# Kernel tuning notes

Hardware: AMD Instinct MI355X
Metric: run time of the kernel (lower is better)

Reference implementation:

```python
import jax, jax.numpy as jnp
import numpy as np

D_MODEL = 1024
STATE_DIM = 64
SEQ_L = 2048


def hippo_legs_A(N):
    n = jnp.arange(N, dtype=jnp.float32)
    two_n1 = 2.0 * n + 1.0
    sq = jnp.sqrt(two_n1[:, None] * two_n1[None, :])
    A = jnp.tril(sq, k=-1) * -1.0
    return A + jnp.diag(-(n + 1.0))


def setup_inputs() -> dict:
    key = jax.random.key(0)
    kB, kC = jax.random.split(key)
    N = STATE_DIM
    n = jnp.arange(N, dtype=jnp.float32)
    B_ref = jnp.sqrt(2.0 * n + 1.0)  # (N,)
    B = jnp.tile(B_ref[None, :], (D_MODEL, 1)) + 0.01 * jax.random.normal(kB, (D_MODEL, N), dtype=jnp.float32)
    C = 0.1 * jax.random.normal(kC, (D_MODEL, N), dtype=jnp.float32)
    D = jnp.zeros((D_MODEL,), dtype=jnp.float32)
    log_dt = jnp.log(jnp.asarray(0.1, dtype=jnp.float32))
    return {"B": B, "C": C, "D": D, "log_dt": log_dt, "L": SEQ_L}


def reference(B, C, D, log_dt, L):
    N = B.shape[1]
    A = hippo_legs_A(N)                       # (N,N) continuous-time HiPPO-LegS
    dt = jax.nn.softplus(log_dt) + 1e-06
    I = jnp.eye(N, dtype=A.dtype)
    lhs = I - 0.5 * dt * A
    rhs = I + 0.5 * dt * A
    A_bar = jnp.linalg.solve(lhs, rhs)        # (N,N) bilinear discretization
    B_bar = jnp.linalg.solve(lhs, (dt * B).T).T  # (d_model, N)
    A_bar_T = A_bar.T

    def step(x, _):
        y = jnp.sum(C * x, axis=-1)           # (d_model,)
        return x @ A_bar_T, y

    _, ys = jax.lax.scan(step, B_bar, None, length=L)  # ys: (L, d_model)
    K = ys.T                                   # (d_model, L)
    K = K.at[:, 0].add(D)
    return K[:, None, :]                       # (d_model, 1, L)
```

## Files before the change

### kernel.cpp

```cpp
#include <hip/hip_runtime.h>

typedef unsigned short ushort_t;
typedef unsigned int uint_t;
typedef short short8 __attribute__((ext_vector_type(8)));
typedef float f32x4 __attribute__((ext_vector_type(4)));

namespace {

template<int CTRL, int RM>
__device__ __forceinline__ float dpp_mov0(float v) {
  return __int_as_float(__builtin_amdgcn_update_dpp(
      0, __float_as_int(v), CTRL, RM, 0xF, false));
}
template<int CTRL, int RM>
__device__ __forceinline__ float dpp_mov1(float v) {
  return __int_as_float(__builtin_amdgcn_update_dpp(
      0x3f800000, __float_as_int(v), CTRL, RM, 0xF, false));
}

__device__ __forceinline__ float rl(float v, int k) {
  return __int_as_float(__builtin_amdgcn_readlane(__float_as_int(v), k));
}

struct Hoist {
  float cs0, cs1, cs2, cs3, cs4, cs5;
  float gs0, gs1, gs2, gs3, gs4, gs5;
  float r, inv_d, hr, alpha, k2;
};

__device__ __forceinline__ Hoist make_hoist(float dt, int n) {
  float h = 0.5f * dt, fn = (float)n;
  float r = sqrtf(2.f * fn + 1.f);
  float d = 1.f + h * (fn + 1.f);
  float inv_d = 1.f / d;
  float g = (1.f - h * fn) * inv_d;
  float c = g - 1.f;
  Hoist H;
  H.r = r; H.inv_d = inv_d; H.hr = h * r;
  H.alpha = 1.f + h * fn;
  H.k2 = r * (2.f - d) * inv_d;
#define COEF_STEP(IDX, CTRL, RM)                                        \
  H.cs##IDX = c; H.gs##IDX = g;                                         \
  { float cP = dpp_mov0<CTRL, RM>(c);                                   \
    float gP = dpp_mov1<CTRL, RM>(g);                                   \
    c = fmaf(g, cP, c); g = g * gP; }
  COEF_STEP(0, 0x111, 0xF)
  COEF_STEP(1, 0x112, 0xF)
  COEF_STEP(2, 0x114, 0xF)
  COEF_STEP(3, 0x118, 0xF)
  COEF_STEP(4, 0x142, 0xA)
  COEF_STEP(5, 0x143, 0xC)
#undef COEF_STEP
  return H;
}

__device__ __forceinline__ float abar_apply(float x, const Hoist& H) {
  float w1 = H.r * x, w2 = H.k2 * x;
#define APPLY_STEP(IDX, CTRL, RM)                                       \
  { float w1P = dpp_mov0<CTRL, RM>(w1);                                 \
    float w2P = dpp_mov0<CTRL, RM>(w2);                                 \
    w2 = fmaf(H.cs##IDX, w1P, fmaf(H.gs##IDX, w2P, w2));                \
    w1 += w1P; }
  APPLY_STEP(0, 0x111, 0xF)
  APPLY_STEP(1, 0x112, 0xF)
  APPLY_STEP(2, 0x114, 0xF)
  APPLY_STEP(3, 0x118, 0xF)
  APPLY_STEP(4, 0x142, 0xA)
  APPLY_STEP(5, 0x143, 0xC)
#undef APPLY_STEP
  float tp = dpp_mov0<0x138, 0xF>(w2);
  return H.inv_d * fmaf(-H.hr, w1 + tp, H.alpha * x);
}

template<int CTRL, int RM>
__device__ __forceinline__ void linrec_step(float& G, float& W) {
  float Wo = dpp_mov0<CTRL, RM>(W);
  float Go = dpp_mov1<CTRL, RM>(G);
  W = fmaf(G, Wo, W);
  G *= Go;
}
__device__ __forceinline__ float lhs_solve(float z, const Hoist& H) {
  float G = H.gs0, W = H.r * z * H.inv_d;
  linrec_step<0x111, 0xF>(G, W);
  linrec_step<0x112, 0xF>(G, W);
  linrec_step<0x114, 0xF>(G, W);
  linrec_step<0x118, 0xF>(G, W);
  linrec_step<0x142, 0xA>(G, W);
  linrec_step<0x143, 0xC>(G, W);
  float sp = dpp_mov0<0x138, 0xF>(W);
  return (z - H.hr * sp) * H.inv_d;
}

__device__ __forceinline__ float softplus_dt(float ldt) {
  return log1pf(expf(ldt)) + 1e-6f;
}

__device__ __forceinline__ void load_row_g(const float* __restrict__ base,
                                           float (&pc)[64]) {
  const float4* p4 = (const float4*)base;
  #pragma unroll
  for (int q = 0; q < 16; ++q) {
    float4 f = p4[q];
    pc[4*q+0] = f.x; pc[4*q+1] = f.y; pc[4*q+2] = f.z; pc[4*q+3] = f.w;
  }
}

__device__ __forceinline__ float qapply(const float (&pc)[64], float u) {
  float a0 = 0.f, a1 = 0.f, a2 = 0.f, a3 = 0.f;
  #pragma unroll
  for (int k = 0; k < 64; k += 4) {
    a0 = fmaf(pc[k + 0], rl(u, k + 0), a0);
    a1 = fmaf(pc[k + 1], rl(u, k + 1), a1);
    a2 = fmaf(pc[k + 2], rl(u, k + 2), a2);
    a3 = fmaf(pc[k + 3], rl(u, k + 3), a3);
  }
  return (a0 + a1) + (a2 + a3);
}

__device__ __forceinline__ float grow_matvec(const float* __restrict__ M,
                                             float u, int lane) {
  float a0 = 0.f, a1 = 0.f, a2 = 0.f, a3 = 0.f;
  const float4* m4 = (const float4*)(M + lane * 64);
  #pragma unroll
  for (int q = 0; q < 16; ++q) {
    float4 f = m4[q];
    a0 = fmaf(f.x, rl(u, 4 * q + 0), a0);
    a1 = fmaf(f.y, rl(u, 4 * q + 1), a1);
    a2 = fmaf(f.z, rl(u, 4 * q + 2), a2);
    a3 = fmaf(f.w, rl(u, 4 * q + 3), a3);
  }
  return (a0 + a1) + (a2 + a3);
}

__device__ __forceinline__ void split_store(float v, ushort_t* Hi,
                                            ushort_t* Lo, int row, int n) {
  uint_t uv = __float_as_uint(v);
  float hf = __uint_as_float(uv & 0xFFFF0000u);
  uint_t lv = __float_as_uint(v - hf);
  int idx = (row << 6) | (((n >> 3) ^ (row & 7)) << 3) | (n & 7);
  Hi[idx] = (ushort_t)(uv >> 16);
  Lo[idx] = (ushort_t)(lv >> 16);
}

__device__ __forceinline__ int frag_off(int row, int chunk) {
  return (row << 6) | ((chunk ^ (row & 7)) << 3);
}

}

__global__ __launch_bounds__(64) void hippo_pow(const float* __restrict__ ldt_p,
                                                float* __restrict__ A32c,
                                                float* __restrict__ QROW,
                                                float* __restrict__ Q2ROW) {
  const int lane = threadIdx.x;
  const int m = blockIdx.x;
  const float dt = softplus_dt(ldt_p[0]);
  const Hoist H = make_hoist(dt, lane);
  float x = (lane == m) ? 1.f : 0.f;
  #pragma unroll 1
  for (int s = 0; s < 32; ++s) x = abar_apply(x, H);
  A32c[lane * 64 + m] = x;
  #pragma unroll 1
  for (int s = 0; s < 32; ++s) x = abar_apply(x, H);
  QROW[m * 64 + lane] = x;
  #pragma unroll 1
  for (int s = 0; s < 64; ++s) x = abar_apply(x, H);
  Q2ROW[m * 64 + lane] = x;
}

__global__ __launch_bounds__(256, 2) void hippo_main(
    const float* __restrict__ B, const float* __restrict__ C,
    const float* __restrict__ Dv, const float* __restrict__ ldt_p,
    const float* __restrict__ A32c, const float* __restrict__ QROW,
    const float* __restrict__ Q2ROW, float* __restrict__ out,
    int NI, int L) {
  __shared__ __align__(16) ushort_t Uh[32 * 64], Ulo[32 * 64];
  __shared__ __align__(16) ushort_t Vh[64 * 64], Vlo[64 * 64];
  const int d = blockIdx.x;
  const int tau = threadIdx.x;
  const int lane = tau & 63;
  const int w = tau >> 6;
  const float dt = softplus_dt(ldt_p[0]);

  if (w == 0) {
    const Hoist H = make_hoist(dt, lane);
    float v = lhs_solve(dt * B[d * 64 + lane], H);
    #pragma unroll 1
    for (int j = 0; j < 32; ++j) {
      split_store(v, Vh, Vlo, j, lane);
      if (j < 31) v = abar_apply(v, H);
    }
  } else if (w == 3) {
    const Hoist H = make_hoist(dt, lane);
    float bb = lhs_solve(dt * B[d * 64 + lane], H);
    float v = grow_matvec(A32c, bb, lane);
    #pragma unroll 1
    for (int j = 32; j < 64; ++j) {
      split_store(v, Vh, Vlo, j, lane);
      if (j < 63) v = abar_apply(v, H);
    }
  } else if (w == 1) {
    float pc[64];
    load_row_g(Q2ROW + lane * 64, pc);
    float u = C[d * 64 + lane];
    #pragma unroll 1
    for (int a = 0; a < 16; ++a) {
      split_store(u, Uh, Ulo, 2 * a, lane);
      if (a < 15) u = qapply(pc, u);
    }
  } else {
    float pc[64];
    load_row_g(Q2ROW + lane * 64, pc);
    float u = grow_matvec(QROW, C[d * 64 + lane], lane);
    #pragma unroll 1
    for (int a = 0; a < 16; ++a) {
      split_store(u, Uh, Ulo, 2 * a + 1, lane);
      if (a < 15) u = qapply(pc, u);
    }
  }
  __syncthreads();

  const int it = w & 1;
  const int jp = w >> 1;
  const int arow = lane & 15;
  const int kg = lane >> 4;
  f32x4 acc0 = {0.f, 0.f, 0.f, 0.f};
  f32x4 acc1 = {0.f, 0.f, 0.f, 0.f};
  const int ia = (it << 4) + arow;
  const int jv0 = (jp << 5) + arow;
  const int jv1 = jv0 + 16;
  #pragma unroll
  for (int k0 = 0; k0 < 2; ++k0) {
    const int ci = (k0 << 2) + kg;
    short8 ah = *(const short8*)&Uh[frag_off(ia, ci)];
    short8 al = *(const short8*)&Ulo[frag_off(ia, ci)];
    short8 b0h = *(const short8*)&Vh[frag_off(jv0, ci)];
    short8 b0l = *(const short8*)&Vlo[frag_off(jv0, ci)];
    short8 b1h = *(const short8*)&Vh[frag_off(jv1, ci)];
    short8 b1l = *(const short8*)&Vlo[frag_off(jv1, ci)];
    acc0 = __builtin_amdgcn_mfma_f32_16x16x32_bf16(ah, b0h, acc0, 0, 0, 0);
    acc0 = __builtin_amdgcn_mfma_f32_16x16x32_bf16(al, b0h, acc0, 0, 0, 0);
    acc0 = __builtin_amdgcn_mfma_f32_16x16x32_bf16(ah, b0l, acc0, 0, 0, 0);
    acc1 = __builtin_amdgcn_mfma_f32_16x16x32_bf16(ah, b1h, acc1, 0, 0, 0);
    acc1 = __builtin_amdgcn_mfma_f32_16x16x32_bf16(al, b1h, acc1, 0, 0, 0);
    acc1 = __builtin_amdgcn_mfma_f32_16x16x32_bf16(ah, b1l, acc1, 0, 0, 0);
  }
  #pragma unroll
  for (int r = 0; r < 4; ++r) {
    const int i = (it << 4) + (kg << 2) + r;
    const int j0 = (jp << 5) + arow;
    float y0 = acc0[r];
    if (i == 0 && j0 == 0) y0 += Dv[d];
    out[((size_t)d << 11) + (i << 6) + j0] = y0;
    out[((size_t)d << 11) + (i << 6) + j0 + 16] = acc1[r];
  }
}

extern "C" void kernel_launch(void* const* d_in, const int* in_sizes, int n_in,
                              void* d_out, int out_size, void* d_ws, size_t ws_size,
                              hipStream_t stream) {
  const float* B   = (const float*)d_in[0];
  const float* C   = (const float*)d_in[1];
  const float* Dv  = (const float*)d_in[2];
  const float* ldt = (const float*)d_in[3];
  const int d_model = in_sizes[2];
  const int L = out_size / d_model;
  const int NI = L / 64;
  float* A32c  = (float*)d_ws;
  float* QROW  = (float*)d_ws + 4096;
  float* Q2ROW = (float*)d_ws + 8192;
  hippo_pow<<<64, 64, 0, stream>>>(ldt, A32c, QROW, Q2ROW);
  hippo_main<<<d_model, 256, 0, stream>>>(B, C, Dv, ldt, A32c, QROW, Q2ROW,
                                          (float*)d_out, NI, L);
}
```

Measured before the change: 39.38 us.

## Split each channel across two blocks by output column half

The grid doubles to two blocks per channel, and each block builds only 32 V vectors (half h uses A^32 times B_bar as its start) instead of 64. The MFMA stage per wave shrinks to one 16x16 tile, and the shared memory for V is halved. This adds parallelism and shortens the serial recurrence chain per block. In exchange, the U (C-side) powers are computed twice per channel, and wave 3 now sits idle during the build phase.

```diff
diff --git a/kernel.cpp b/kernel.cpp
--- a/kernel.cpp
+++ b/kernel.cpp
@@ -172,11 +172,11 @@
     const float* __restrict__ B, const float* __restrict__ C,
     const float* __restrict__ Dv, const float* __restrict__ ldt_p,
     const float* __restrict__ A32c, const float* __restrict__ QROW,
-    const float* __restrict__ Q2ROW, float* __restrict__ out,
-    int NI, int L) {
+    const float* __restrict__ Q2ROW, float* __restrict__ out) {
   __shared__ __align__(16) ushort_t Uh[32 * 64], Ulo[32 * 64];
-  __shared__ __align__(16) ushort_t Vh[64 * 64], Vlo[64 * 64];
-  const int d = blockIdx.x;
+  __shared__ __align__(16) ushort_t Vh[32 * 64], Vlo[32 * 64];
+  const int d = blockIdx.x >> 1;
+  const int h = blockIdx.x & 1;
   const int tau = threadIdx.x;
   const int lane = tau & 63;
   const int w = tau >> 6;
@@ -185,19 +185,11 @@
   if (w == 0) {
     const Hoist H = make_hoist(dt, lane);
     float v = lhs_solve(dt * B[d * 64 + lane], H);
+    if (h) v = grow_matvec(A32c, v, lane);
     #pragma unroll 1
     for (int j = 0; j < 32; ++j) {
       split_store(v, Vh, Vlo, j, lane);
       if (j < 31) v = abar_apply(v, H);
-    }
-  } else if (w == 3) {
-    const Hoist H = make_hoist(dt, lane);
-    float bb = lhs_solve(dt * B[d * 64 + lane], H);
-    float v = grow_matvec(A32c, bb, lane);
-    #pragma unroll 1
-    for (int j = 32; j < 64; ++j) {
-      split_store(v, Vh, Vlo, j, lane);
-      if (j < 63) v = abar_apply(v, H);
     }
   } else if (w == 1) {
     float pc[64];
@@ -208,7 +200,7 @@
       split_store(u, Uh, Ulo, 2 * a, lane);
       if (a < 15) u = qapply(pc, u);
     }
-  } else {
+  } else if (w == 2) {
     float pc[64];
     load_row_g(Q2ROW + lane * 64, pc);
     float u = grow_matvec(QROW, C[d * 64 + lane], lane);
@@ -221,38 +213,30 @@
   __syncthreads();
 
   const int it = w & 1;
-  const int jp = w >> 1;
+  const int jt = w >> 1;
   const int arow = lane & 15;
   const int kg = lane >> 4;
-  f32x4 acc0 = {0.f, 0.f, 0.f, 0.f};
-  f32x4 acc1 = {0.f, 0.f, 0.f, 0.f};
+  f32x4 acc = {0.f, 0.f, 0.f, 0.f};
   const int ia = (it << 4) + arow;
-  const int jv0 = (jp << 5) + arow;
-  const int jv1 = jv0 + 16;
+  const int jv = (jt << 4) + arow;
   #pragma unroll
   for (int k0 = 0; k0 < 2; ++k0) {
     const int ci = (k0 << 2) + kg;
     short8 ah = *(const short8*)&Uh[frag_off(ia, ci)];
     short8 al = *(const short8*)&Ulo[frag_off(ia, ci)];
-    short8 b0h = *(const short8*)&Vh[frag_off(jv0, ci)];
-    short8 b0l = *(const short8*)&Vlo[frag_off(jv0, ci)];
-    short8 b1h = *(const short8*)&Vh[frag_off(jv1, ci)];
-    short8 b1l = *(const short8*)&Vlo[frag_off(jv1, ci)];
-    acc0 = __builtin_amdgcn_mfma_f32_16x16x32_bf16(ah, b0h, acc0, 0, 0, 0);
-    acc0 = __builtin_amdgcn_mfma_f32_16x16x32_bf16(al, b0h, acc0, 0, 0, 0);
-    acc0 = __builtin_amdgcn_mfma_f32_16x16x32_bf16(ah, b0l, acc0, 0, 0, 0);
-    acc1 = __builtin_amdgcn_mfma_f32_16x16x32_bf16(ah, b1h, acc1, 0, 0, 0);
-    acc1 = __builtin_amdgcn_mfma_f32_16x16x32_bf16(al, b1h, acc1, 0, 0, 0);
-    acc1 = __builtin_amdgcn_mfma_f32_16x16x32_bf16(ah, b1l, acc1, 0, 0, 0);
+    short8 bh = *(const short8*)&Vh[frag_off(jv, ci)];
+    short8 bl = *(const short8*)&Vlo[frag_off(jv, ci)];
+    acc = __builtin_amdgcn_mfma_f32_16x16x32_bf16(ah, bh, acc, 0, 0, 0);
+    acc = __builtin_amdgcn_mfma_f32_16x16x32_bf16(al, bh, acc, 0, 0, 0);
+    acc = __builtin_amdgcn_mfma_f32_16x16x32_bf16(ah, bl, acc, 0, 0, 0);
   }
   #pragma unroll
   for (int r = 0; r < 4; ++r) {
     const int i = (it << 4) + (kg << 2) + r;
-    const int j0 = (jp << 5) + arow;
-    float y0 = acc0[r];
-    if (i == 0 && j0 == 0) y0 += Dv[d];
-    out[((size_t)d << 11) + (i << 6) + j0] = y0;
-    out[((size_t)d << 11) + (i << 6) + j0 + 16] = acc1[r];
+    const int jg = (h << 5) + (jt << 4) + arow;
+    float y = acc[r];
+    if (i == 0 && jg == 0) y += Dv[d];
+    out[((size_t)d << 11) + (i << 6) + jg] = y;
   }
 }
 
@@ -264,12 +248,10 @@
   const float* Dv  = (const float*)d_in[2];
   const float* ldt = (const float*)d_in[3];
   const int d_model = in_sizes[2];
-  const int L = out_size / d_model;
-  const int NI = L / 64;
   float* A32c  = (float*)d_ws;
   float* QROW  = (float*)d_ws + 4096;
   float* Q2ROW = (float*)d_ws + 8192;
   hippo_pow<<<64, 64, 0, stream>>>(ldt, A32c, QROW, Q2ROW);
-  hippo_main<<<d_model, 256, 0, stream>>>(B, C, Dv, ldt, A32c, QROW, Q2ROW,
-                                          (float*)d_out, NI, L);
-}
+  hippo_main<<<2 * d_model, 256, 0, stream>>>(B, C, Dv, ldt, A32c, QROW, Q2ROW,
+                                              (float*)d_out);
+}
```

After: 48.94 us. +24.3%, slower.

## Replace per-channel serial recurrences with precomputed matrix powers and batched GEMMs

Applied to the files above, without the earlier changes.

Precomputes all powers A_bar^1..63 and powers of A_bar^64 in small kernels, then computes the V and U sequences for all channels with a batched split-bf16 MFMA GEMM instead of serial per-channel matvec chains. The final output kernel reads V/U from global workspace instead of shared memory. This aims to remove the long serial dependency chain inside each block, at the cost of four launches, much larger workspace traffic (tens of MB written and re-read) and serial chains kept in the prep kernels.

```diff
diff --git a/kernel.cpp b/kernel.cpp
--- a/kernel.cpp
+++ b/kernel.cpp
@@ -117,127 +117,167 @@
   return (a0 + a1) + (a2 + a3);
 }
 
-__device__ __forceinline__ float grow_matvec(const float* __restrict__ M,
-                                             float u, int lane) {
-  float a0 = 0.f, a1 = 0.f, a2 = 0.f, a3 = 0.f;
-  const float4* m4 = (const float4*)(M + lane * 64);
-  #pragma unroll
-  for (int q = 0; q < 16; ++q) {
-    float4 f = m4[q];
-    a0 = fmaf(f.x, rl(u, 4 * q + 0), a0);
-    a1 = fmaf(f.y, rl(u, 4 * q + 1), a1);
-    a2 = fmaf(f.z, rl(u, 4 * q + 2), a2);
-    a3 = fmaf(f.w, rl(u, 4 * q + 3), a3);
-  }
-  return (a0 + a1) + (a2 + a3);
-}
-
-__device__ __forceinline__ void split_store(float v, ushort_t* Hi,
-                                            ushort_t* Lo, int row, int n) {
+__device__ __forceinline__ void bsplit(float v, ushort_t& h, ushort_t& l) {
   uint_t uv = __float_as_uint(v);
   float hf = __uint_as_float(uv & 0xFFFF0000u);
   uint_t lv = __float_as_uint(v - hf);
-  int idx = (row << 6) | (((n >> 3) ^ (row & 7)) << 3) | (n & 7);
-  Hi[idx] = (ushort_t)(uv >> 16);
-  Lo[idx] = (ushort_t)(lv >> 16);
-}
-
-__device__ __forceinline__ int frag_off(int row, int chunk) {
-  return (row << 6) | ((chunk ^ (row & 7)) << 3);
-}
-
-}
-
-__global__ __launch_bounds__(64) void hippo_pow(const float* __restrict__ ldt_p,
-                                                float* __restrict__ A32c,
-                                                float* __restrict__ QROW,
-                                                float* __restrict__ Q2ROW) {
+  h = (ushort_t)(uv >> 16);
+  l = (ushort_t)(lv >> 16);
+}
+
+}
+
+__global__ __launch_bounds__(64) void hippo_prep(
+    const float* __restrict__ B, const float* __restrict__ C,
+    const float* __restrict__ ldt_p, float* __restrict__ AjRM,
+    float* __restrict__ PRM, ushort_t* __restrict__ Bh, ushort_t* __restrict__ Bl,
+    ushort_t* __restrict__ Ch, ushort_t* __restrict__ Cl,
+    ushort_t* __restrict__ Vh, ushort_t* __restrict__ Vl,
+    ushort_t* __restrict__ Uh, ushort_t* __restrict__ Ul) {
+  const int lane = threadIdx.x;
+  const int bid = blockIdx.x;
+  const float dt = softplus_dt(ldt_p[0]);
+  const Hoist H = make_hoist(dt, lane);
+  if (bid < 64) {
+    const int m = bid;
+    float x = (lane == m) ? 1.f : 0.f;
+    #pragma unroll 1
+    for (int s = 1; s <= 64; ++s) {
+      x = abar_apply(x, H);
+      if (s < 64) AjRM[s * 4096 + lane * 64 + m] = x;
+      else        PRM[lane * 64 + m] = x;
+    }
+  } else {
+    const int d = bid - 64;
+    float bb = lhs_solve(dt * B[d * 64 + lane], H);
+    ushort_t h, l;
+    bsplit(bb, h, l);
+    Bh[d * 64 + lane] = h;               Bl[d * 64 + lane] = l;
+    Vh[(size_t)d * 4096 + lane] = h;     Vl[(size_t)d * 4096 + lane] = l;
+    float cc = C[d * 64 + lane];
+    bsplit(cc, h, l);
+    Ch[d * 64 + lane] = h;               Cl[d * 64 + lane] = l;
+    Uh[(size_t)d * 2048 + lane] = h;     Ul[(size_t)d * 2048 + lane] = l;
+  }
+}
+
+__global__ __launch_bounds__(64) void hippo_ppow(const float* __restrict__ PRM,
+                                                 float* __restrict__ PiT) {
   const int lane = threadIdx.x;
   const int m = blockIdx.x;
-  const float dt = softplus_dt(ldt_p[0]);
-  const Hoist H = make_hoist(dt, lane);
-  float x = (lane == m) ? 1.f : 0.f;
+  float pc[64];
+  load_row_g(PRM + lane * 64, pc);
+  float x = PRM[lane * 64 + m];
+  PiT[4096 + m * 64 + lane] = x;
   #pragma unroll 1
-  for (int s = 0; s < 32; ++s) x = abar_apply(x, H);
-  A32c[lane * 64 + m] = x;
-  #pragma unroll 1
-  for (int s = 0; s < 32; ++s) x = abar_apply(x, H);
-  QROW[m * 64 + lane] = x;
-  #pragma unroll 1
-  for (int s = 0; s < 64; ++s) x = abar_apply(x, H);
-  Q2ROW[m * 64 + lane] = x;
-}
-
-__global__ __launch_bounds__(256, 2) void hippo_main(
-    const float* __restrict__ B, const float* __restrict__ C,
-    const float* __restrict__ Dv, const float* __restrict__ ldt_p,
-    const float* __restrict__ A32c, const float* __restrict__ QROW,
-    const float* __restrict__ Q2ROW, float* __restrict__ out,
-    int NI, int L) {
-  __shared__ __align__(16) ushort_t Uh[32 * 64], Ulo[32 * 64];
-  __shared__ __align__(16) ushort_t Vh[64 * 64], Vlo[64 * 64];
+  for (int i = 2; i <= 31; ++i) {
+    x = qapply(pc, x);
+    PiT[i * 4096 + m * 64 + lane] = x;
+  }
+}
+
+__global__ __launch_bounds__(256) void hippo_gemm(
+    const ushort_t* __restrict__ Bh, const ushort_t* __restrict__ Bl,
+    const ushort_t* __restrict__ Ch, const ushort_t* __restrict__ Cl,
+    const float* __restrict__ AjRM, const float* __restrict__ PiT,
+    ushort_t* __restrict__ Vh, ushort_t* __restrict__ Vl,
+    ushort_t* __restrict__ Uh, ushort_t* __restrict__ Ul, int MT) {
+  __shared__ __align__(16) float Bs[64 * 64];
+  const int s = blockIdx.x / MT;
+  const int mt = blockIdx.x % MT;
+  const int tau = threadIdx.x;
+  const int lane = tau & 63;
+  const int w = tau >> 6;
+  const bool isV = (s < 63);
+  const int j = isV ? (s + 1) : (s - 62);
+  const float* Msrc = isV ? (AjRM + j * 4096) : (PiT + j * 4096);
+  const ushort_t* Ah = isV ? Bh : Ch;
+  const ushort_t* Al = isV ? Bl : Cl;
+
+  #pragma unroll
+  for (int p = 0; p < 4; ++p) {
+    const int idx = tau + 256 * p;
+    const int row = idx >> 4, c4 = idx & 15;
+    f32x4 f = *(const f32x4*)(Msrc + idx * 4);
+    *(f32x4*)&Bs[row * 64 + ((c4 ^ (row & 15)) << 2)] = f;
+  }
+  __syncthreads();
+
+  const int arow = lane & 15, kg = lane >> 4;
+  const int drow = mt * 64 + w * 16 + arow;
+  f32x4 acc0 = {0.f,0.f,0.f,0.f}, acc1 = {0.f,0.f,0.f,0.f};
+  f32x4 acc2 = {0.f,0.f,0.f,0.f}, acc3 = {0.f,0.f,0.f,0.f};
+  #pragma unroll
+  for (int k0 = 0; k0 < 2; ++k0) {
+    const size_t aoff = (size_t)drow * 64 + k0 * 32 + kg * 8;
+    short8 ah = *(const short8*)(Ah + aoff);
+    short8 al = *(const short8*)(Al + aoff);
+    #pragma unroll
+    for (int nt = 0; nt < 4; ++nt) {
+      const int nrow = nt * 16 + arow;
+      const int c4a = k0 * 8 + kg * 2;
+      f32x4 f0 = *(const f32x4*)&Bs[nrow * 64 + ((c4a ^ (nrow & 15)) << 2)];
+      f32x4 f1 = *(const f32x4*)&Bs[nrow * 64 + (((c4a + 1) ^ (nrow & 15)) << 2)];
+      short8 bh, bl;
+      #pragma unroll
+      for (int e = 0; e < 4; ++e) {
+        ushort_t hh, ll;
+        bsplit(f0[e], hh, ll); bh[e] = (short)hh; bl[e] = (short)ll;
+        bsplit(f1[e], hh, ll); bh[4 + e] = (short)hh; bl[4 + e] = (short)ll;
+      }
+      f32x4 a = (nt == 0) ? acc0 : (nt == 1) ? acc1 : (nt == 2) ? acc2 : acc3;
+      a = __builtin_amdgcn_mfma_f32_16x16x32_bf16(ah, bh, a, 0, 0, 0);
+      a = __builtin_amdgcn_mfma_f32_16x16x32_bf16(al, bh, a, 0, 0, 0);
+      a = __builtin_amdgcn_mfma_f32_16x16x32_bf16(ah, bl, a, 0, 0, 0);
+      if (nt == 0) acc0 = a; else if (nt == 1) acc1 = a;
+      else if (nt == 2) acc2 = a; else acc3 = a;
+    }
+  }
+  ushort_t* Oh = isV ? Vh : Uh;
+  ushort_t* Ol = isV ? Vl : Ul;
+  const int jd = isV ? 64 : 32;
+  #pragma unroll
+  for (int nt = 0; nt < 4; ++nt) {
+    f32x4 a = (nt == 0) ? acc0 : (nt == 1) ? acc1 : (nt == 2) ? acc2 : acc3;
+    #pragma unroll
+    for (int r = 0; r < 4; ++r) {
+      const int dd = mt * 64 + w * 16 + kg * 4 + r;
+      const int nn = nt * 16 + arow;
+      const size_t off = ((size_t)dd * jd + j) * 64 + nn;
+      ushort_t hh, ll;
+      bsplit(a[r], hh, ll);
+      Oh[off] = hh;
+      Ol[off] = ll;
+    }
+  }
+}
+
+__global__ __launch_bounds__(256) void hippo_out(
+    const float* __restrict__ Dv,
+    const ushort_t* __restrict__ Uh, const ushort_t* __restrict__ Ul,
+    const ushort_t* __restrict__ Vh, const ushort_t* __restrict__ Vl,
+    float* __restrict__ out) {
   const int d = blockIdx.x;
   const int tau = threadIdx.x;
   const int lane = tau & 63;
   const int w = tau >> 6;
-  const float dt = softplus_dt(ldt_p[0]);
-
-  if (w == 0) {
-    const Hoist H = make_hoist(dt, lane);
-    float v = lhs_solve(dt * B[d * 64 + lane], H);
-    #pragma unroll 1
-    for (int j = 0; j < 32; ++j) {
-      split_store(v, Vh, Vlo, j, lane);
-      if (j < 31) v = abar_apply(v, H);
-    }
-  } else if (w == 3) {
-    const Hoist H = make_hoist(dt, lane);
-    float bb = lhs_solve(dt * B[d * 64 + lane], H);
-    float v = grow_matvec(A32c, bb, lane);
-    #pragma unroll 1
-    for (int j = 32; j < 64; ++j) {
-      split_store(v, Vh, Vlo, j, lane);
-      if (j < 63) v = abar_apply(v, H);
-    }
-  } else if (w == 1) {
-    float pc[64];
-    load_row_g(Q2ROW + lane * 64, pc);
-    float u = C[d * 64 + lane];
-    #pragma unroll 1
-    for (int a = 0; a < 16; ++a) {
-      split_store(u, Uh, Ulo, 2 * a, lane);
-      if (a < 15) u = qapply(pc, u);
-    }
-  } else {
-    float pc[64];
-    load_row_g(Q2ROW + lane * 64, pc);
-    float u = grow_matvec(QROW, C[d * 64 + lane], lane);
-    #pragma unroll 1
-    for (int a = 0; a < 16; ++a) {
-      split_store(u, Uh, Ulo, 2 * a + 1, lane);
-      if (a < 15) u = qapply(pc, u);
-    }
-  }
-  __syncthreads();
-
-  const int it = w & 1;
-  const int jp = w >> 1;
-  const int arow = lane & 15;
-  const int kg = lane >> 4;
-  f32x4 acc0 = {0.f, 0.f, 0.f, 0.f};
-  f32x4 acc1 = {0.f, 0.f, 0.f, 0.f};
+  const int it = w & 1, jp = w >> 1;
+  const int arow = lane & 15, kg = lane >> 4;
+  f32x4 acc0 = {0.f,0.f,0.f,0.f}, acc1 = {0.f,0.f,0.f,0.f};
   const int ia = (it << 4) + arow;
   const int jv0 = (jp << 5) + arow;
   const int jv1 = jv0 + 16;
+  const size_t ub = (size_t)d * 2048;
+  const size_t vb = (size_t)d * 4096;
   #pragma unroll
   for (int k0 = 0; k0 < 2; ++k0) {
-    const int ci = (k0 << 2) + kg;
-    short8 ah = *(const short8*)&Uh[frag_off(ia, ci)];
-    short8 al = *(const short8*)&Ulo[frag_off(ia, ci)];
-    short8 b0h = *(const short8*)&Vh[frag_off(jv0, ci)];
-    short8 b0l = *(const short8*)&Vlo[frag_off(jv0, ci)];
-    short8 b1h = *(const short8*)&Vh[frag_off(jv1, ci)];
-    short8 b1l = *(const short8*)&Vlo[frag_off(jv1, ci)];
+    const int ko = k0 * 32 + kg * 8;
+    short8 ah  = *(const short8*)(Uh + ub + ia * 64 + ko);
+    short8 al  = *(const short8*)(Ul + ub + ia * 64 + ko);
+    short8 b0h = *(const short8*)(Vh + vb + jv0 * 64 + ko);
+    short8 b0l = *(const short8*)(Vl + vb + jv0 * 64 + ko);
+    short8 b1h = *(const short8*)(Vh + vb + jv1 * 64 + ko);
+    short8 b1l = *(const short8*)(Vl + vb + jv1 * 64 + ko);
     acc0 = __builtin_amdgcn_mfma_f32_16x16x32_bf16(ah, b0h, acc0, 0, 0, 0);
     acc0 = __builtin_amdgcn_mfma_f32_16x16x32_bf16(al, b0h, acc0, 0, 0, 0);
     acc0 = __builtin_amdgcn_mfma_f32_16x16x32_bf16(ah, b0l, acc0, 0, 0, 0);
@@ -264,12 +304,26 @@
   const float* Dv  = (const float*)d_in[2];
   const float* ldt = (const float*)d_in[3];
   const int d_model = in_sizes[2];
-  const int L = out_size / d_model;
-  const int NI = L / 64;
-  float* A32c  = (float*)d_ws;
-  float* QROW  = (float*)d_ws + 4096;
-  float* Q2ROW = (float*)d_ws + 8192;
-  hippo_pow<<<64, 64, 0, stream>>>(ldt, A32c, QROW, Q2ROW);
-  hippo_main<<<d_model, 256, 0, stream>>>(B, C, Dv, ldt, A32c, QROW, Q2ROW,
-                                          (float*)d_out, NI, L);
-}
+  const int MT = d_model / 64;
+
+  char* ws = (char*)d_ws;
+  size_t o = 0;
+  float* AjRM = (float*)(ws + o); o += (size_t)64 * 4096 * 4;
+  float* PRM  = (float*)(ws + o); o += 4096 * 4;
+  float* PiT  = (float*)(ws + o); o += (size_t)32 * 4096 * 4;
+  ushort_t* Bh = (ushort_t*)(ws + o); o += (size_t)d_model * 64 * 2;
+  ushort_t* Bl = (ushort_t*)(ws + o); o += (size_t)d_model * 64 * 2;
+  ushort_t* Ch = (ushort_t*)(ws + o); o += (size_t)d_model * 64 * 2;
+  ushort_t* Cl = (ushort_t*)(ws + o); o += (size_t)d_model * 64 * 2;
+  ushort_t* Vh = (ushort_t*)(ws + o); o += (size_t)d_model * 4096 * 2;
+  ushort_t* Vl = (ushort_t*)(ws + o); o += (size_t)d_model * 4096 * 2;
+  ushort_t* Uh = (ushort_t*)(ws + o); o += (size_t)d_model * 2048 * 2;
+  ushort_t* Ul = (ushort_t*)(ws + o); o += (size_t)d_model * 2048 * 2;
+
+  hippo_prep<<<64 + d_model, 64, 0, stream>>>(B, C, ldt, AjRM, PRM,
+                                              Bh, Bl, Ch, Cl, Vh, Vl, Uh, Ul);
+  hippo_ppow<<<64, 64, 0, stream>>>(PRM, PiT);
+  hippo_gemm<<<94 * MT, 256, 0, stream>>>(Bh, Bl, Ch, Cl, AjRM, PiT,
+                                          Vh, Vl, Uh, Ul, MT);
+  hippo_out<<<d_model, 256, 0, stream>>>(Dv, Uh, Ul, Vh, Vl, (float*)d_out);
+}
```

New measurement: 49.55 us. 1.26x slower.
